# Optimization experiments

Measured on AMD Instinct MI355X. Metric: run time of the kernel, lower is better.

## Reference

```python
import jax, jax.numpy as jnp
import numpy as np

# ---- model hyperparameters (match init_kwargs) ----
NUM_INPUT, NUM_HIDDEN, NUM_OUTPUT = 2048, 65536, 512
FAN_OUT = 256
TAU, THRESHOLD = 20.0, 0.3
SPIKE_DELAY = 1  # must be 1 for the one-step-delay scan formulation below
N = NUM_INPUT + NUM_HIDDEN + NUM_OUTPUT
HID_START, OUT_START = NUM_INPUT, NUM_INPUT + NUM_HIDDEN
SURROGATE_SCALE = 25.0


@jax.custom_vjp
def spike(v):
    """Heaviside spike with sigmoid surrogate gradient (SurrogateSpike)."""
    return (v >= THRESHOLD).astype(v.dtype)

def _spike_fwd(v):
    return spike(v), v

def _spike_bwd(v, g):
    s = jax.nn.sigmoid(SURROGATE_SCALE * (v - THRESHOLD))
    return (g * SURROGATE_SCALE * s * (1.0 - s),)

spike.defvjp(_spike_fwd, _spike_bwd)


def make_targets(seed=42):
    """Structured random connectivity (mirrors _generate_random_targets ranges)."""
    rng = np.random.default_rng(seed)
    t = np.empty((N, FAN_OUT), dtype=np.int64)
    # input neurons -> hidden
    t[:NUM_INPUT] = rng.integers(HID_START, OUT_START, size=(NUM_INPUT, FAN_OUT))
    # hidden neurons -> hidden+output, excluding self
    hid = rng.integers(HID_START, N, size=(NUM_HIDDEN, FAN_OUT))
    src = np.arange(HID_START, OUT_START)[:, None]
    R = N - HID_START
    hid = np.where(hid == src, HID_START + (hid - HID_START + 1) % R, hid)
    t[HID_START:OUT_START] = hid
    # output neurons -> hidden
    t[OUT_START:] = rng.integers(HID_START, OUT_START, size=(NUM_OUTPUT, FAN_OUT))
    return jnp.asarray(t, dtype=jnp.int32)


def setup_inputs() -> dict:
    key = jax.random.key(0)
    k1, k2 = jax.random.split(key)
    weights = jax.random.normal(k1, (N, FAN_OUT), dtype=jnp.float32) * 0.3
    input_spikes = jax.random.bernoulli(k2, 0.2, (NUM_INPUT,))
    return {"input_spikes": input_spikes, "weights": weights,
            "targets": make_targets(), "max_timesteps": 50}


def _simulate(input_spikes, weights, targets, max_timesteps):
    decay_base = jnp.exp(jnp.float32(-1.0 / TAU))
    idx = jnp.arange(N)
    flat_targets = targets.reshape(-1)  # [N*FAN_OUT]

    inp = jnp.zeros(N, bool).at[:NUM_INPUT].set(input_spikes)
    pot = jnp.zeros(N, jnp.float32)
    last_update = jnp.zeros(N, jnp.int32)
    has_fired = inp
    strength = jnp.where(inp, 2.0, 0.0).astype(jnp.float32)
    out_times = jnp.full(NUM_OUTPUT, -1, jnp.int32)
    fire_now = inp  # input spikes scheduled on the wheel at t=0

    def step(carry, t):
        pot, last_update, has_fired, strength, fire_now, out_times = carry
        # contributions of spiking sources: spike_strength[src] * weights[src]
        src_val = jnp.where(fire_now, strength, 0.0)                 # [N]
        contrib = (src_val[:, None] * weights).reshape(-1)           # [N*FAN_OUT]
        # neurons that receive at least one spike this step (the 'unique_targets')
        hits = jnp.zeros(N, jnp.float32).at[flat_targets].add(
            jnp.repeat(fire_now.astype(jnp.float32), FAN_OUT))
        is_target = hits > 0
        # lazy retroactive decay only on touched neurons
        dt = (t - last_update).astype(jnp.float32)
        pot = jnp.where(is_target, pot * decay_base ** dt, pot)
        last_update = jnp.where(is_target, t, last_update)
        # scatter-add contributions (zeros for non-firing sources)
        pot = pot.at[flat_targets].add(contrib)
        # spike check with refractory mask
        probs = spike(pot) * (1.0 - has_fired.astype(jnp.float32))
        new_fired = probs > 0.5
        has_fired = has_fired | new_fired
        strength = jnp.where(new_fired, probs, strength)
        out_times = jnp.where(new_fired[OUT_START:] & (out_times < 0), t, out_times)
        # schedule hidden spikes for delivery at t + 1 (spike_delay == 1)
        fire_next = new_fired & (idx < OUT_START)
        # reset membrane of newly fired non-output neurons
        reset = jnp.where(idx >= OUT_START, 0.0, probs)
        pot = pot * (1.0 - reset)
        return (pot, last_update, has_fired, strength, fire_next, out_times), None

    carry = (pot, last_update, has_fired, strength, fire_now, out_times)
    carry, _ = jax.lax.scan(step, carry, jnp.arange(max_timesteps, dtype=jnp.int32))
    pot, last_update, has_fired, strength, _, out_times = carry
    # final decay to end of simulation window
    final_dt = (max_timesteps - last_update).astype(jnp.float32)
    pot = pot * decay_base ** final_dt
    return out_times, pot[OUT_START:]


def reference(input_spikes, weights, targets, max_timesteps):
    out_times, out_pot = _simulate(input_spikes, weights, targets, max_timesteps)
    return out_times, out_pot
```

## Files before the change

### kernel.cpp

```cpp
#include <hip/hip_runtime.h>
#include <math.h>

#define N_TOTAL    68096
#define NUM_INPUT  2048
#define NUM_OUTPUT 512
#define OUT_START  67584
#define N_TGT      66048
#define NUM_HIDDEN 65536
#define FB_WORDS   2048
#define FAN_OUT    256
#define THRESH     0.3f
#define T_MAX      50
#define T_BIG      12
#define BM_WORDS   2064
#define LIST_CAP   12288

#define QTR_SZ     16512
#define N_CHUNK    128
#define DENSE_THR  6000


__device__ __forceinline__ int calc_chunks(int fcnt) {
    int c = fcnt >> 7;
    if (c < 1) c = 1;
    if (c > N_CHUNK) c = N_CHUNK;
    return c;
}

__global__ __launch_bounds__(256) void init_k(
    const unsigned int* __restrict__ in0,
    float* pot, float* acc, int* last_up, unsigned char* fired,
    int* frontier0, int* cnt, float* out_f, float* decay_tab,
    unsigned* fbits)
{
    __shared__ int sF, sG;
    const int tid = threadIdx.x;
    if (tid == 0) { sF = 0; sG = 0; }
    __syncthreads();
    for (int k = tid; k < 512; k += 256) {
        unsigned int v = in0[k];
        if (v == 0x3F800000u) atomicAdd(&sF, 1);
        else if (v > 1u)      sG = 1;
    }
    __syncthreads();
    const int mode = (sF >= 8) ? 1 : (sG ? 2 : 0);

    const int i = blockIdx.x * 256 + tid;
    const int lane = tid & 63;
    if (i <= T_MAX) {
        float base = expf(-0.05f);
        decay_tab[i] = (float)pow((double)base, (double)i);
    }
    if (i < NUM_OUTPUT) out_f[i] = -1.0f;
    if (i < FB_WORDS)   fbits[i] = 0u;
    bool want = false;
    if (i < N_TOTAL) {
        pot[i] = 0.0f;
        acc[i] = 0.0f;
        last_up[i] = 0;
        bool s = false;
        if (i < NUM_INPUT) {
            if (mode == 0)      s = ((const int*)in0)[i] != 0;
            else if (mode == 1) s = ((const float*)in0)[i] != 0.0f;
            else                s = ((const unsigned char*)in0)[i] != 0;
        }
        fired[i] = s ? 1 : 0;
        want = s;
    }
    unsigned long long m = __ballot(want);
    if (m) {
        int leader = __ffsll((long long)m) - 1;
        int base = 0;
        if (lane == leader) base = atomicAdd(&cnt[0], __popcll(m));
        base = __shfl(base, leader, 64);
        if (want) {
            int off = __popcll(m & ((1ull << (unsigned)lane) - 1ull));
            frontier0[base + off] = i;
        }
    }
}

#define LIVE(SFB, TG) ({ int b_ = (TG) - NUM_INPUT; \
    (b_ >= NUM_HIDDEN) || !((SFB[b_ >> 5] >> (b_ & 31)) & 1u); })

__global__ __launch_bounds__(1024) void step_scatter_k(
    const int* __restrict__ fr, const int* __restrict__ cnt_cur,
    int* cnt_next,
    const int* __restrict__ targets, const float* __restrict__ weights,
    float* __restrict__ acc, float* __restrict__ rep,
    const unsigned* __restrict__ fbits)
{
    __shared__ float    lacc[QTR_SZ];
    __shared__ unsigned sfb[FB_WORDS];
    const int fcnt = *cnt_cur;
    const int tid  = threadIdx.x;
    if (blockIdx.x == 0 && tid == 0) *cnt_next = 0;
    if (fcnt == 0) return;

    if (fcnt < DENSE_THR) {
        const int nq = fcnt * (FAN_OUT / 4);
        const int q  = blockIdx.x * 1024 + tid;
        if (blockIdx.x * 1024 >= nq) return;
        for (int k = tid; k < FB_WORDS; k += 1024) sfb[k] = fbits[k];
        __syncthreads();
        if (q < nq) {
            int s  = fr[q >> 6];
            int j4 = (q & 63) << 2;
            const int base = s * FAN_OUT + j4;
            int4 tg = *(const int4*)(targets + base);
            const bool lx = LIVE(sfb, tg.x), ly = LIVE(sfb, tg.y);
            const bool lz = LIVE(sfb, tg.z), lw = LIVE(sfb, tg.w);
            if (lx | ly | lz | lw) {
                float4 wv = *(const float4*)(weights + base);
                float  st = (s < NUM_INPUT) ? 2.0f : 1.0f;
                if (lx) atomicAdd(&acc[tg.x], st * wv.x);
                if (ly) atomicAdd(&acc[tg.y], st * wv.y);
                if (lz) atomicAdd(&acc[tg.z], st * wv.z);
                if (lw) atomicAdd(&acc[tg.w], st * wv.w);
            }
        }
        return;
    }

    const int chunks = calc_chunks(fcnt);
    const int c   = blockIdx.x & 127;
    const int qtr = blockIdx.x >> 7;
    if (c >= chunks) return;
    for (int k = tid; k < FB_WORDS; k += 1024) sfb[k] = fbits[k];
    const int base = NUM_INPUT + qtr * QTR_SZ;
    for (int k = tid; k < QTR_SZ / 4; k += 1024)
        ((float4*)lacc)[k] = make_float4(0.f, 0.f, 0.f, 0.f);
    __syncthreads();
    const int lo = (int)(((long long)fcnt * c)       / chunks);
    const int hi = (int)(((long long)fcnt * (c + 1)) / chunks);
    const int nq = (hi - lo) << 6;
    for (int q = tid; q < nq; q += 2048) {
        const int q2 = q + 1024;
        const bool hasB = q2 < nq;
        const int sA  = fr[lo + (q >> 6)];
        const int sB  = hasB ? fr[lo + (q2 >> 6)] : sA;
        const int ebA = sA * FAN_OUT + ((q  & 63) << 2);
        const int ebB = sB * FAN_OUT + ((q2 & 63) << 2);
        int4 tgA = *(const int4*)(targets + ebA);
        int4 tgB = *(const int4*)(targets + ebB);
        {
            int x = tgA.x - base; const bool kx = (unsigned)x < QTR_SZ && LIVE(sfb, tgA.x);
            int y = tgA.y - base; const bool ky = (unsigned)y < QTR_SZ && LIVE(sfb, tgA.y);
            int z = tgA.z - base; const bool kz = (unsigned)z < QTR_SZ && LIVE(sfb, tgA.z);
            int u = tgA.w - base; const bool ku = (unsigned)u < QTR_SZ && LIVE(sfb, tgA.w);
            if (kx | ky | kz | ku) {
                float4 wv = *(const float4*)(weights + ebA);
                const float st = (sA < NUM_INPUT) ? 2.0f : 1.0f;
                if (kx) atomicAdd(&lacc[x], st * wv.x);
                if (ky) atomicAdd(&lacc[y], st * wv.y);
                if (kz) atomicAdd(&lacc[z], st * wv.z);
                if (ku) atomicAdd(&lacc[u], st * wv.w);
            }
        }
        if (hasB) {
            int x = tgB.x - base; const bool kx = (unsigned)x < QTR_SZ && LIVE(sfb, tgB.x);
            int y = tgB.y - base; const bool ky = (unsigned)y < QTR_SZ && LIVE(sfb, tgB.y);
            int z = tgB.z - base; const bool kz = (unsigned)z < QTR_SZ && LIVE(sfb, tgB.z);
            int u = tgB.w - base; const bool ku = (unsigned)u < QTR_SZ && LIVE(sfb, tgB.w);
            if (kx | ky | kz | ku) {
                float4 wv = *(const float4*)(weights + ebB);
                const float st = (sB < NUM_INPUT) ? 2.0f : 1.0f;
                if (kx) atomicAdd(&lacc[x], st * wv.x);
                if (ky) atomicAdd(&lacc[y], st * wv.y);
                if (kz) atomicAdd(&lacc[z], st * wv.z);
                if (ku) atomicAdd(&lacc[u], st * wv.w);
            }
        }
    }
    __syncthreads();
    float4* out = (float4*)(rep + (size_t)((c << 2) + qtr) * QTR_SZ);
    for (int k = tid; k < QTR_SZ / 4; k += 1024) out[k] = ((float4*)lacc)[k];
}

__global__ __launch_bounds__(128) void step_update_k(
    const float* __restrict__ rep, const int* __restrict__ cnt_cur,
    float* __restrict__ pot, float* __restrict__ acc,
    int* __restrict__ last_up, unsigned char* __restrict__ fired,
    int* __restrict__ frontier_next, int* __restrict__ cnt_next,
    float* __restrict__ out_f, const float* __restrict__ decay_tab, int t,
    unsigned* __restrict__ fbits)
{
    const int fcnt = *cnt_cur;
    if (fcnt == 0) return;
    const int g = blockIdx.x * 128 + threadIdx.x;
    const int lane = threadIdx.x & 63;
    bool w2 = false;
    const int n = NUM_INPUT + g;
    if (n >= OUT_START || !fired[n]) {
        float a;
        if (fcnt < DENSE_THR) {
            a = acc[n];
            if (a != 0.0f) acc[n] = 0.0f;
        } else {
            const int chunks = calc_chunks(fcnt);
            const int qtr = g / QTR_SZ;
            const int idx = g - qtr * QTR_SZ;
            const float* p0 = rep + (size_t)qtr * QTR_SZ + idx;
            float a0 = 0.f, a1 = 0.f, a2 = 0.f, a3 = 0.f;
            int c = 0;
            for (; c + 3 < chunks; c += 4) {
                a0 += p0[(size_t)(c + 0) * (4 * QTR_SZ)];
                a1 += p0[(size_t)(c + 1) * (4 * QTR_SZ)];
                a2 += p0[(size_t)(c + 2) * (4 * QTR_SZ)];
                a3 += p0[(size_t)(c + 3) * (4 * QTR_SZ)];
            }
            for (; c < chunks; ++c)
                a0 += p0[(size_t)c * (4 * QTR_SZ)];
            a = (a0 + a1) + (a2 + a3);
        }
        if (a != 0.0f) {
            float p = pot[n] * decay_tab[t - last_up[n]] + a;
            last_up[n] = t;
            if (!fired[n] && p >= THRESH) {
                fired[n] = 1;
                if (n < OUT_START) {
                    p = 0.0f; w2 = true;
                    const int b = n - NUM_INPUT;
                    atomicOr(&fbits[b >> 5], 1u << (b & 31));
                } else out_f[n - OUT_START] = (float)t;
            }
            pot[n] = p;
        }
    }
    unsigned long long m = __ballot(w2);
    if (m) {
        int leader = __ffsll((long long)m) - 1;
        int base = 0;
        if (lane == leader) base = atomicAdd(cnt_next, __popcll(m));
        base = __shfl(base, leader, 64);
        if (w2) {
            int off = __popcll(m & ((1ull << (unsigned)lane) - 1ull));
            frontier_next[base + off] = n;
        }
    }
}

__global__ __launch_bounds__(1024) void tail_k(
    float* __restrict__ pot, float* __restrict__ acc,
    int* __restrict__ last_up, unsigned char* __restrict__ fired,
    int* __restrict__ fr0, int* __restrict__ fr1, int* __restrict__ cnt,
    const int* __restrict__ targets, const float* __restrict__ weights,
    float* __restrict__ out_f, const float* __restrict__ decay_tab,
    const unsigned* __restrict__ fbits)
{
    __shared__ unsigned bm[BM_WORDS];
    __shared__ unsigned sfb[FB_WORDS];
    __shared__ int      lst[LIST_CAP];
    __shared__ int      lcnt, ovf;
    __shared__ float    sdecay[T_MAX + 1];
    const int tid = threadIdx.x;
    if (tid <= T_MAX) sdecay[tid] = decay_tab[tid];
    for (int k = tid; k < FB_WORDS; k += 1024) sfb[k] = fbits[k];

    for (int t = T_BIG; t < T_MAX; ++t) {
        const int cur = t & 1, nxt = cur ^ 1;
        for (int k = tid; k < BM_WORDS; k += 1024) bm[k] = 0u;
        if (tid == 0) { lcnt = 0; ovf = 0; cnt[nxt] = 0; }
        __syncthreads();
        const int fcnt = cnt[cur];
        if (fcnt == 0) break;
        const int* fr  = (cur == 0) ? fr0 : fr1;
        int*       frn = (cur == 0) ? fr1 : fr0;

        const int nq = fcnt * (FAN_OUT / 4);
        for (int q = tid; q < nq; q += 1024) {
            int s  = fr[q >> 6];
            int j4 = (q & 63) << 2;
            const int base = s * FAN_OUT + j4;
            int4 tg = *(const int4*)(targets + base);
            const bool lx = LIVE(sfb, tg.x), ly = LIVE(sfb, tg.y);
            const bool lz = LIVE(sfb, tg.z), lw = LIVE(sfb, tg.w);
            if (!(lx | ly | lz | lw)) continue;
            float4 wv = *(const float4*)(weights + base);
            float  st = (s < NUM_INPUT) ? 2.0f : 1.0f;
            #define EDGE(L, TG, WV) if (L) {                                  \
                atomicAdd(&acc[TG], st * (WV));                               \
                int b = (TG) - NUM_INPUT;                                     \
                unsigned bit = 1u << (b & 31);                                \
                unsigned old = atomicOr(&bm[b >> 5], bit);                    \
                if (!(old & bit)) {                                           \
                    int p_ = atomicAdd(&lcnt, 1);                             \
                    if (p_ < LIST_CAP) lst[p_] = (TG); else ovf = 1;          \
                } }
            EDGE(lx, tg.x, wv.x); EDGE(ly, tg.y, wv.y);
            EDGE(lz, tg.z, wv.z); EDGE(lw, tg.w, wv.w);
            #undef EDGE
        }
        __syncthreads();

        const int M = lcnt;
        const bool full = (ovf != 0);
        const int lo = full ? (NUM_INPUT + tid) : tid;
        const int hi = full ? N_TOTAL : M;
        for (int k = lo; k < hi; k += 1024) {
            const int n = full ? k : lst[k];
            if (n < OUT_START && fired[n]) continue;
            float a = __hip_atomic_load(&acc[n], __ATOMIC_RELAXED,
                                        __HIP_MEMORY_SCOPE_AGENT);
            if (a != 0.0f) {
                __hip_atomic_store(&acc[n], 0.0f, __ATOMIC_RELAXED,
                                   __HIP_MEMORY_SCOPE_AGENT);
                float p = pot[n] * sdecay[t - last_up[n]] + a;
                last_up[n] = t;
                if (!fired[n] && p >= THRESH) {
                    fired[n] = 1;
                    if (n < OUT_START) {
                        p = 0.0f;
                        int pos = atomicAdd(&cnt[nxt], 1);
                        frn[pos] = n;
                        const int b = n - NUM_INPUT;
                        atomicOr(&sfb[b >> 5], 1u << (b & 31));
                    } else out_f[n - OUT_START] = (float)t;
                }
                pot[n] = p;
            }
        }
        __syncthreads();
    }

    __syncthreads();
    for (int i = tid; i < NUM_OUTPUT; i += 1024) {
        int n = OUT_START + i;
        out_f[NUM_OUTPUT + i] = pot[n] * sdecay[T_MAX - last_up[n]];
    }
}

extern "C" void kernel_launch(void* const* d_in, const int* in_sizes, int n_in,
                              void* d_out, int out_size, void* d_ws, size_t ws_size,
                              hipStream_t stream) {
    const void*  in_spikes = d_in[0];
    const float* weights   = (const float*)d_in[1];
    const int*   targets   = (const int*)d_in[2];
    float*       out_f     = (float*)d_out;

    char* w = (char*)d_ws;
    int*      cnt       = (int*)w;
    float*    decay_tab = (float*)(w + 256);
    float*    pot       = (float*)(w + 512);
    float*    acc       = pot + N_TOTAL;
    int*      last_up   = (int*)(acc + N_TOTAL);
    int*      fr0       = last_up + N_TOTAL;
    int*      fr1       = fr0 + N_TOTAL;
    unsigned* fbits     = (unsigned*)(fr1 + N_TOTAL);
    unsigned char* fired = (unsigned char*)(fbits + FB_WORDS);
    size_t base_bytes = (size_t)((char*)(fired + N_TOTAL) - w);
    size_t rep_off    = (base_bytes + 255) & ~(size_t)255;
    float* rep        = (float*)(w + rep_off);

    hipMemsetAsync(cnt, 0, 16, stream);
    init_k<<<266, 256, 0, stream>>>((const unsigned int*)in_spikes,
                                    pot, acc, last_up, fired,
                                    fr0, cnt, out_f, decay_tab, fbits);

    int* fr[2] = {fr0, fr1};
    for (int t = 0; t < T_BIG; ++t) {
        const int cur = t & 1, nxt = cur ^ 1;
        step_scatter_k<<<4 * N_CHUNK, 1024, 0, stream>>>(
            fr[cur], &cnt[cur], &cnt[nxt], targets, weights, acc, rep, fbits);
        step_update_k<<<516, 128, 0, stream>>>(
            rep, &cnt[cur], pot, acc, last_up, fired,
            fr[nxt], &cnt[nxt], out_f, decay_tab, t, fbits);
    }
    tail_k<<<1, 1024, 0, stream>>>(pot, acc, last_up, fired, fr0, fr1, cnt,
                                   targets, weights, out_f, decay_tab, fbits);
}
```

Measured before the change: 264.9 us.

## Gate dense scatter path on frontier size times unfired neurons, grid-stride sparse path

Replaces the fixed frontier-count threshold for choosing the dense per-chunk replica path with a product of frontier size and remaining unfired hidden neurons, tracked with an extra counter updated by atomics. This keeps the sparse atomic path active longer once most targets have fired and are filtered out. The sparse path becomes a grid-stride loop so it can cover frontiers larger than the grid. Replica writes and reads also use nontemporal stores and loads to reduce cache pollution. The trade-off is more global atomics on the contended sparse path at larger frontiers, plus an extra atomic per wave.

```diff
diff --git a/kernel.cpp b/kernel.cpp
--- a/kernel.cpp
+++ b/kernel.cpp
@@ -17,7 +17,9 @@
 
 #define QTR_SZ     16512
 #define N_CHUNK    128
-#define DENSE_THR  6000
+#define DENSE_K    2000
+
+typedef float v4f __attribute__((ext_vector_type(4)));
 
 
 __device__ __forceinline__ int calc_chunks(int fcnt) {
@@ -25,6 +27,10 @@
     if (c < 1) c = 1;
     if (c > N_CHUNK) c = N_CHUNK;
     return c;
+}
+
+__device__ __forceinline__ bool gate_dense(int fcnt, int unfired) {
+    return (long long)fcnt * unfired >= (long long)DENSE_K * NUM_HIDDEN;
 }
 
 __global__ __launch_bounds__(256) void init_k(
@@ -47,6 +53,7 @@
 
     const int i = blockIdx.x * 256 + tid;
     const int lane = tid & 63;
+    if (i == 0) cnt[2] = NUM_HIDDEN;
     if (i <= T_MAX) {
         float base = expf(-0.05f);
         decay_tab[i] = (float)pow((double)base, (double)i);
@@ -85,25 +92,29 @@
 
 __global__ __launch_bounds__(1024) void step_scatter_k(
     const int* __restrict__ fr, const int* __restrict__ cnt_cur,
-    int* cnt_next,
+    int* cnt_next, const int* __restrict__ unf_cur, int* unf_next,
     const int* __restrict__ targets, const float* __restrict__ weights,
     float* __restrict__ acc, float* __restrict__ rep,
     const unsigned* __restrict__ fbits)
 {
     __shared__ float    lacc[QTR_SZ];
     __shared__ unsigned sfb[FB_WORDS];
-    const int fcnt = *cnt_cur;
+    const int fcnt    = *cnt_cur;
+    const int unfired = *unf_cur;
     const int tid  = threadIdx.x;
-    if (blockIdx.x == 0 && tid == 0) *cnt_next = 0;
+    if (blockIdx.x == 0 && tid == 0) {
+        *cnt_next = 0;
+        *unf_next = unfired;
+    }
     if (fcnt == 0) return;
 
-    if (fcnt < DENSE_THR) {
+    if (!gate_dense(fcnt, unfired)) {
         const int nq = fcnt * (FAN_OUT / 4);
-        const int q  = blockIdx.x * 1024 + tid;
         if (blockIdx.x * 1024 >= nq) return;
         for (int k = tid; k < FB_WORDS; k += 1024) sfb[k] = fbits[k];
         __syncthreads();
-        if (q < nq) {
+        const int stride = gridDim.x * 1024;
+        for (int q = blockIdx.x * 1024 + tid; q < nq; q += stride) {
             int s  = fr[q >> 6];
             int j4 = (q & 63) << 2;
             const int base = s * FAN_OUT + j4;
@@ -173,12 +184,15 @@
         }
     }
     __syncthreads();
-    float4* out = (float4*)(rep + (size_t)((c << 2) + qtr) * QTR_SZ);
-    for (int k = tid; k < QTR_SZ / 4; k += 1024) out[k] = ((float4*)lacc)[k];
+    v4f* out = (v4f*)(rep + (size_t)((c << 2) + qtr) * QTR_SZ);
+    const v4f* lv = (const v4f*)lacc;
+    for (int k = tid; k < QTR_SZ / 4; k += 1024)
+        __builtin_nontemporal_store(lv[k], &out[k]);
 }
 
 __global__ __launch_bounds__(128) void step_update_k(
     const float* __restrict__ rep, const int* __restrict__ cnt_cur,
+    const int* __restrict__ unf_cur, int* unf_next,
     float* __restrict__ pot, float* __restrict__ acc,
     int* __restrict__ last_up, unsigned char* __restrict__ fired,
     int* __restrict__ frontier_next, int* __restrict__ cnt_next,
@@ -187,13 +201,14 @@
 {
     const int fcnt = *cnt_cur;
     if (fcnt == 0) return;
+    const int unfired = *unf_cur;
     const int g = blockIdx.x * 128 + threadIdx.x;
     const int lane = threadIdx.x & 63;
     bool w2 = false;
     const int n = NUM_INPUT + g;
     if (n >= OUT_START || !fired[n]) {
         float a;
-        if (fcnt < DENSE_THR) {
+        if (!gate_dense(fcnt, unfired)) {
             a = acc[n];
             if (a != 0.0f) acc[n] = 0.0f;
         } else {
@@ -204,13 +219,13 @@
             float a0 = 0.f, a1 = 0.f, a2 = 0.f, a3 = 0.f;
             int c = 0;
             for (; c + 3 < chunks; c += 4) {
-                a0 += p0[(size_t)(c + 0) * (4 * QTR_SZ)];
-                a1 += p0[(size_t)(c + 1) * (4 * QTR_SZ)];
-                a2 += p0[(size_t)(c + 2) * (4 * QTR_SZ)];
-                a3 += p0[(size_t)(c + 3) * (4 * QTR_SZ)];
+                a0 += __builtin_nontemporal_load(&p0[(size_t)(c + 0) * (4 * QTR_SZ)]);
+                a1 += __builtin_nontemporal_load(&p0[(size_t)(c + 1) * (4 * QTR_SZ)]);
+                a2 += __builtin_nontemporal_load(&p0[(size_t)(c + 2) * (4 * QTR_SZ)]);
+                a3 += __builtin_nontemporal_load(&p0[(size_t)(c + 3) * (4 * QTR_SZ)]);
             }
             for (; c < chunks; ++c)
-                a0 += p0[(size_t)c * (4 * QTR_SZ)];
+                a0 += __builtin_nontemporal_load(&p0[(size_t)c * (4 * QTR_SZ)]);
             a = (a0 + a1) + (a2 + a3);
         }
         if (a != 0.0f) {
@@ -231,7 +246,11 @@
     if (m) {
         int leader = __ffsll((long long)m) - 1;
         int base = 0;
-        if (lane == leader) base = atomicAdd(cnt_next, __popcll(m));
+        if (lane == leader) {
+            const int cntw = __popcll(m);
+            base = atomicAdd(cnt_next, cntw);
+            atomicSub(unf_next, cntw);
+        }
         base = __shfl(base, leader, 64);
         if (w2) {
             int off = __popcll(m & ((1ull << (unsigned)lane) - 1ull));
@@ -352,7 +371,7 @@
     size_t rep_off    = (base_bytes + 255) & ~(size_t)255;
     float* rep        = (float*)(w + rep_off);
 
-    hipMemsetAsync(cnt, 0, 16, stream);
+    (void)hipMemsetAsync(cnt, 0, 16, stream);
     init_k<<<266, 256, 0, stream>>>((const unsigned int*)in_spikes,
                                     pot, acc, last_up, fired,
                                     fr0, cnt, out_f, decay_tab, fbits);
@@ -360,10 +379,12 @@
     int* fr[2] = {fr0, fr1};
     for (int t = 0; t < T_BIG; ++t) {
         const int cur = t & 1, nxt = cur ^ 1;
+        const int ucur = 2 + (t & 1), unxt = 2 + ((t + 1) & 1);
         step_scatter_k<<<4 * N_CHUNK, 1024, 0, stream>>>(
-            fr[cur], &cnt[cur], &cnt[nxt], targets, weights, acc, rep, fbits);
+            fr[cur], &cnt[cur], &cnt[nxt], &cnt[ucur], &cnt[unxt],
+            targets, weights, acc, rep, fbits);
         step_update_k<<<516, 128, 0, stream>>>(
-            rep, &cnt[cur], pot, acc, last_up, fired,
+            rep, &cnt[cur], &cnt[ucur], &cnt[unxt], pot, acc, last_up, fired,
             fr[nxt], &cnt[nxt], out_f, decay_tab, t, fbits);
     }
     tail_k<<<1, 1024, 0, stream>>>(pot, acc, last_up, fired, fr0, fr1, cnt,
```

Result: slower. 334.6 us (+26.4%).
